# Optimization experiments

Hardware: AMD Instinct MI355X
Metric: run time of the kernel (lower is better)

## Reference

```python
import jax, jax.numpy as jnp
import numpy as np

N, E, D, H = 50000, 800000, 64, 64  # nodes, edges, feat dim, hidden dim
EPS = 1e-3  # Keras BatchNormalization default epsilon

def bn(x, g, b, mu, v):
    # inference-mode batch norm with moving statistics
    return (x - mu) * jax.lax.rsqrt(v + EPS) * g + b

def gelu(x):
    return jax.nn.gelu(x, approximate=False)  # tf.nn.gelu default is exact

def setup_inputs() -> dict:
    key = jax.random.key(0)
    ks = jax.random.split(key, 24)
    r = lambda i, shape, s=1.0: (jax.random.normal(ks[i], shape, jnp.float32) * s)
    inp = {
        "node_feats": r(0, (N, D)),
        "edge_feats": r(1, (E, D)),
        "src": jax.random.randint(ks[2], (E,), 0, N, jnp.int32),
        "dst": jax.random.randint(ks[3], (E,), 0, N, jnp.int32),
        # message MLP (BN -> Dense(gelu)) x2, input D
        "m_g1": 1.0 + 0.1 * r(4, (D,)), "m_b1": 0.1 * r(5, (D,)),
        "m_mu1": 0.1 * r(6, (D,)), "m_v1": jnp.ones((D,), jnp.float32),
        "m_W1": r(7, (D, H), 1.0 / np.sqrt(D)), "m_c1": jnp.zeros((H,), jnp.float32),
        "m_g2": 1.0 + 0.1 * r(8, (H,)), "m_b2": 0.1 * r(9, (H,)),
        "m_mu2": 0.1 * r(10, (H,)), "m_v2": jnp.ones((H,), jnp.float32),
        "m_W2": r(11, (H, H), 1.0 / np.sqrt(H)), "m_c2": jnp.zeros((H,), jnp.float32),
        # edge transformer MLP (Dense(gelu)) x2, input D
        "e_W1": r(12, (D, H), 1.0 / np.sqrt(D)), "e_c1": jnp.zeros((H,), jnp.float32),
        "e_W2": r(13, (H, H), 1.0 / np.sqrt(H)), "e_c2": jnp.zeros((H,), jnp.float32),
        # update MLP (BN -> Dense(gelu)) x2, input D+H (concat combination)
        "u_g1": 1.0 + 0.1 * r(14, (D + H,)), "u_b1": 0.1 * r(15, (D + H,)),
        "u_mu1": 0.1 * r(16, (D + H,)), "u_v1": jnp.ones((D + H,), jnp.float32),
        "u_W1": r(17, (D + H, H), 1.0 / np.sqrt(D + H)), "u_c1": jnp.zeros((H,), jnp.float32),
        "u_g2": 1.0 + 0.1 * r(18, (H,)), "u_b2": 0.1 * r(19, (H,)),
        "u_mu2": 0.1 * r(20, (H,)), "u_v2": jnp.ones((H,), jnp.float32),
        "u_W2": r(21, (H, H), 1.0 / np.sqrt(H)), "u_c2": jnp.zeros((H,), jnp.float32),
    }
    return inp

def reference(node_feats, edge_feats,
              m_g1, m_b1, m_mu1, m_v1, m_W1, m_c1,
              m_g2, m_b2, m_mu2, m_v2, m_W2, m_c2,
              e_W1, e_c1, e_W2, e_c2,
              u_g1, u_b1, u_mu1, u_v1, u_W1, u_c1,
              u_g2, u_b2, u_mu2, u_v2, u_W2, u_c2,
              src, dst):
    # gather neighbour representations: [E, D]
    nbr = node_feats[dst]
    # base message MLP: (BN -> Dropout(identity at inference) -> Dense gelu) x2
    h = gelu(bn(nbr, m_g1, m_b1, m_mu1, m_v1) @ m_W1 + m_c1)
    msg = gelu(bn(h, m_g2, m_b2, m_mu2, m_v2) @ m_W2 + m_c2)
    # edge transformer: Dense(gelu) x2, gates the messages elementwise
    er = gelu(edge_feats @ e_W1 + e_c1)
    er = gelu(er @ e_W2 + e_c2)
    msg = msg * er  # [E, H]
    # unsorted_segment_mean over source node indices (empty segments -> 0)
    s = jax.ops.segment_sum(msg, src, num_segments=N)
    cnt = jax.ops.segment_sum(jnp.ones((E, 1), msg.dtype), src, num_segments=N)
    agg = s / jnp.maximum(cnt, 1.0)  # [N, H]
    # combine ('concat') and update MLP
    hcat = jnp.concatenate([node_feats, agg], axis=-1)  # [N, D+H]
    h = gelu(bn(hcat, u_g1, u_b1, u_mu1, u_v1) @ u_W1 + u_c1)
    out = gelu(bn(h, u_g2, u_b2, u_mu2, u_v2) @ u_W2 + u_c2)
    return out  # [N, H]
```

## Files before the change

### kernel.cpp

```cpp
#include <hip/hip_runtime.h>
#include <hip/hip_bf16.h>

#define NN 50000
#define NE 800000

typedef __bf16 bf16_t;
typedef bf16_t bf16x8 __attribute__((ext_vector_type(8)));
typedef float f32x4 __attribute__((ext_vector_type(4)));

__device__ __forceinline__ float gelu_f(float x) {
    float v = x * fmaf(x * x, 0.07135481627f, 1.595769122f);
    float e = __expf(-v);
    return x * __builtin_amdgcn_rcpf(1.0f + e);
}

__device__ void fold_frag(int K, const float* W, const float* g, const float* b,
                          const float* mu, const float* v, const float* c,
                          bf16_t* Wf, float* cb, int n) {
    float acc = c[n];
    const int nt = n >> 4, lrow = n & 15, nkc = K >> 5;
    for (int k = 0; k < K; ++k) {
        float w = W[k * 64 + n];
        float s = 1.0f, o = 0.0f;
        if (g) {
            s = g[k] * __frsqrt_rn(v[k] + 1e-3f);
            o = b[k] - mu[k] * s;
        }
        int idx = ((nt * nkc + (k >> 5)) * 64 + ((k >> 3) & 3) * 16 + lrow) * 8 + (k & 7);
        Wf[idx] = (bf16_t)(w * s);
        acc += o * w;
    }
    cb[n] = acc;
}

__global__ void fold_kernel(
    const float* mg1, const float* mb1, const float* mmu1, const float* mv1,
    const float* mW1, const float* mc1,
    const float* mg2, const float* mb2, const float* mmu2, const float* mv2,
    const float* mW2, const float* mc2,
    const float* eW1, const float* ec1, const float* eW2, const float* ec2,
    const float* ug1, const float* ub1, const float* umu1, const float* uv1,
    const float* uW1, const float* uc1,
    const float* ug2, const float* ub2, const float* umu2, const float* uv2,
    const float* uW2, const float* uc2,
    bf16_t* wcat,
    bf16_t* uW1f, bf16_t* uW2f,
    float* cm1, float* cm2, float* ce1, float* ce2, float* cu1, float* cu2)
{
    int n = threadIdx.x;
    if (n >= 64) return;
    switch (blockIdx.x) {
        case 0: fold_frag(64,  mW1, mg1, mb1, mmu1, mv1, mc1, wcat,         cm1, n); break;
        case 1: fold_frag(64,  mW2, mg2, mb2, mmu2, mv2, mc2, wcat + 4096,  cm2, n); break;
        case 2: fold_frag(64,  eW1, nullptr, nullptr, nullptr, nullptr, ec1, wcat + 8192,  ce1, n); break;
        case 3: fold_frag(64,  eW2, nullptr, nullptr, nullptr, nullptr, ec2, wcat + 12288, ce2, n); break;
        case 4: fold_frag(128, uW1, ug1, ub1, umu1, uv1, uc1, uW1f, cu1, n); break;
        case 5: fold_frag(64,  uW2, ug2, ub2, umu2, uv2, uc2, uW2f, cu2, n); break;
    }
}

__device__ __forceinline__ void mk_frag_hilo(const float* row, int quad,
        bf16x8& hi0, bf16x8& lo0, bf16x8& hi1, bf16x8& lo1)
{
    #pragma unroll
    for (int j = 0; j < 8; ++j) {
        float x0 = row[quad * 8 + j];
        float x1 = row[32 + quad * 8 + j];
        bf16_t h0 = (bf16_t)x0, h1 = (bf16_t)x1;
        hi0[j] = h0; lo0[j] = (bf16_t)(x0 - (float)h0);
        hi1[j] = h1; lo1[j] = (bf16_t)(x1 - (float)h1);
    }
}

__device__ __forceinline__ bf16x8 ldb(const bf16_t* wf, int slot, int lane) {
    return *(const bf16x8*)(wf + (slot * 64 + lane) * 8);
}

__device__ __forceinline__ void gemm64_hilo(const bf16_t* wf, int m,
        bf16x8 h0, bf16x8 l0, bf16x8 h1, bf16x8 l1, f32x4 (&acc)[4], int lane)
{
    #pragma unroll
    for (int nt = 0; nt < 4; ++nt) {
        bf16x8 b0 = ldb(wf, m * 8 + nt * 2 + 0, lane);
        bf16x8 b1 = ldb(wf, m * 8 + nt * 2 + 1, lane);
        f32x4 c = {0.f, 0.f, 0.f, 0.f};
        c = __builtin_amdgcn_mfma_f32_16x16x32_bf16(h0, b0, c, 0, 0, 0);
        c = __builtin_amdgcn_mfma_f32_16x16x32_bf16(l0, b0, c, 0, 0, 0);
        c = __builtin_amdgcn_mfma_f32_16x16x32_bf16(h1, b1, c, 0, 0, 0);
        c = __builtin_amdgcn_mfma_f32_16x16x32_bf16(l1, b1, c, 0, 0, 0);
        acc[nt] = c;
    }
}

__device__ __forceinline__ void gemm64(const bf16_t* wf, int m,
        bf16x8 a0, bf16x8 a1, f32x4 (&acc)[4], int lane)
{
    #pragma unroll
    for (int nt = 0; nt < 4; ++nt) {
        bf16x8 b0 = ldb(wf, m * 8 + nt * 2 + 0, lane);
        bf16x8 b1 = ldb(wf, m * 8 + nt * 2 + 1, lane);
        f32x4 c = {0.f, 0.f, 0.f, 0.f};
        c = __builtin_amdgcn_mfma_f32_16x16x32_bf16(a0, b0, c, 0, 0, 0);
        c = __builtin_amdgcn_mfma_f32_16x16x32_bf16(a1, b1, c, 0, 0, 0);
        acc[nt] = c;
    }
}

__device__ __forceinline__ void epi_to_frag(const f32x4 (&acc)[4], const float* bias,
        bf16_t* h, int lrow, int quad)
{
    #pragma unroll
    for (int nt = 0; nt < 4; ++nt) {
        float bb = bias[nt * 16 + lrow];
        #pragma unroll
        for (int r = 0; r < 4; ++r)
            h[((nt * 2 + (lrow >> 3)) * 16 + quad * 4 + r) * 8 + (lrow & 7)] =
                (bf16_t)gelu_f(acc[nt][r] + bb);
    }
}

__global__ __launch_bounds__(256) void edge_kernel(
    const float* __restrict__ node_feats, const float* __restrict__ edge_feats,
    const int* __restrict__ src, const int* __restrict__ dst,
    const bf16_t* __restrict__ wcat,
    const float* __restrict__ cm1, const float* __restrict__ cm2,
    const float* __restrict__ ce1, const float* __restrict__ ce2,
    float* __restrict__ s_acc, int* __restrict__ cnt)
{
    __shared__ bf16_t wf[16384];
    __shared__ bf16_t hf[4][1024];

    const int tid  = threadIdx.x;
    const int wave = tid >> 6;
    const int lane = tid & 63;
    const int quad = lane >> 4;
    const int lrow = lane & 15;

    #pragma unroll
    for (int i = 0; i < 8; ++i) {
        int chunk = tid + i * 256;
        *(bf16x8*)(wf + chunk * 8) = *(const bf16x8*)(wcat + chunk * 8);
    }
    __syncthreads();

    const int ebase = blockIdx.x * 64 + wave * 16;
    bf16_t* h = hf[wave];

    if (quad == 0) atomicAdd(&cnt[src[ebase + lrow]], 1);

    f32x4 acc[4];

    {
        const float* erow = edge_feats + (size_t)(ebase + lrow) * 64;
        bf16x8 h0, l0, h1, l1;
        mk_frag_hilo(erow, quad, h0, l0, h1, l1);
        gemm64_hilo(wf, 2, h0, l0, h1, l1, acc, lane);
        epi_to_frag(acc, ce1, h, lrow, quad);
    }
    float er[4][4];
    {
        bf16x8 a0 = *(const bf16x8*)(h + lane * 8);
        bf16x8 a1 = *(const bf16x8*)(h + (lane + 64) * 8);
        gemm64(wf, 3, a0, a1, acc, lane);
        #pragma unroll
        for (int nt = 0; nt < 4; ++nt) {
            float bb = ce2[nt * 16 + lrow];
            #pragma unroll
            for (int r = 0; r < 4; ++r) er[nt][r] = gelu_f(acc[nt][r] + bb);
        }
    }

    {
        const int dnode = dst[ebase + lrow];
        const float* nrow = node_feats + (size_t)dnode * 64;
        bf16x8 h0, l0, h1, l1;
        mk_frag_hilo(nrow, quad, h0, l0, h1, l1);
        gemm64_hilo(wf, 0, h0, l0, h1, l1, acc, lane);
        epi_to_frag(acc, cm1, h, lrow, quad);
    }
    float msg[4][4];
    {
        bf16x8 a0 = *(const bf16x8*)(h + lane * 8);
        bf16x8 a1 = *(const bf16x8*)(h + (lane + 64) * 8);
        gemm64(wf, 1, a0, a1, acc, lane);
        #pragma unroll
        for (int nt = 0; nt < 4; ++nt) {
            float bb = cm2[nt * 16 + lrow];
            #pragma unroll
            for (int r = 0; r < 4; ++r) msg[nt][r] = gelu_f(acc[nt][r] + bb);
        }
    }

    #pragma unroll
    for (int r = 0; r < 4; ++r) {
        float* srow = s_acc + (size_t)src[ebase + quad * 4 + r] * 64;
        #pragma unroll
        for (int nt = 0; nt < 4; ++nt)
            unsafeAtomicAdd(srow + nt * 16 + lrow, msg[nt][r] * er[nt][r]);
    }
}

__global__ __launch_bounds__(256) void node_kernel(
    const float* __restrict__ node_feats,
    const float* __restrict__ s_acc, const int* __restrict__ cnt,
    const bf16_t* __restrict__ uW1f, const float* __restrict__ cu1,
    const bf16_t* __restrict__ uW2f, const float* __restrict__ cu2,
    float* __restrict__ out)
{
    __shared__ bf16_t w1f[8192];
    __shared__ bf16_t w2f[4096];
    __shared__ bf16_t hf[4][1024];

    const int tid  = threadIdx.x;
    const int wave = tid >> 6;
    const int lane = tid & 63;
    const int quad = lane >> 4;
    const int lrow = lane & 15;

    #pragma unroll
    for (int i = 0; i < 4; ++i) {
        int chunk = tid + i * 256;
        *(bf16x8*)(w1f + chunk * 8) = *(const bf16x8*)(uW1f + chunk * 8);
    }
    #pragma unroll
    for (int i = 0; i < 2; ++i) {
        int chunk = tid + i * 256;
        *(bf16x8*)(w2f + chunk * 8) = *(const bf16x8*)(uW2f + chunk * 8);
    }
    __syncthreads();

    const int nbase = blockIdx.x * 64 + wave * 16;
    int arow = nbase + lrow;
    arow = arow < NN ? arow : NN - 1;

    const float* nf   = node_feats + (size_t)arow * 64;
    const float* srow = s_acc + (size_t)arow * 64;
    float inv = 1.0f / fmaxf((float)cnt[arow], 1.0f);

    bf16x8 ah[4], al[4];
    #pragma unroll
    for (int j = 0; j < 8; ++j) {
        float x0 = nf[quad * 8 + j];
        float x1 = nf[32 + quad * 8 + j];
        float x2 = srow[quad * 8 + j] * inv;
        float x3 = srow[32 + quad * 8 + j] * inv;
        bf16_t h0 = (bf16_t)x0, h1 = (bf16_t)x1, h2 = (bf16_t)x2, h3 = (bf16_t)x3;
        ah[0][j] = h0; al[0][j] = (bf16_t)(x0 - (float)h0);
        ah[1][j] = h1; al[1][j] = (bf16_t)(x1 - (float)h1);
        ah[2][j] = h2; al[2][j] = (bf16_t)(x2 - (float)h2);
        ah[3][j] = h3; al[3][j] = (bf16_t)(x3 - (float)h3);
    }

    f32x4 acc[4];
    #pragma unroll
    for (int nt = 0; nt < 4; ++nt) {
        f32x4 c = {0.f, 0.f, 0.f, 0.f};
        #pragma unroll
        for (int kk = 0; kk < 4; ++kk) {
            bf16x8 b = *(const bf16x8*)(w1f + ((nt * 4 + kk) * 64 + lane) * 8);
            c = __builtin_amdgcn_mfma_f32_16x16x32_bf16(ah[kk], b, c, 0, 0, 0);
            c = __builtin_amdgcn_mfma_f32_16x16x32_bf16(al[kk], b, c, 0, 0, 0);
        }
        acc[nt] = c;
    }
    bf16_t* hb = hf[wave];
    epi_to_frag(acc, cu1, hb, lrow, quad);

    bf16x8 ha0 = *(const bf16x8*)(hb + lane * 8);
    bf16x8 ha1 = *(const bf16x8*)(hb + (lane + 64) * 8);
    gemm64(w2f, 0, ha0, ha1, acc, lane);

    #pragma unroll
    for (int nt = 0; nt < 4; ++nt) {
        int col = nt * 16 + lrow;
        float bb = cu2[col];
        #pragma unroll
        for (int r = 0; r < 4; ++r) {
            int row = nbase + quad * 4 + r;
            if (row < NN)
                out[(size_t)row * 64 + col] = gelu_f(acc[nt][r] + bb);
        }
    }
}

extern "C" void kernel_launch(void* const* d_in, const int* in_sizes, int n_in,
                              void* d_out, int out_size, void* d_ws, size_t ws_size,
                              hipStream_t stream) {
    const float* node_feats = (const float*)d_in[0];
    const float* edge_feats = (const float*)d_in[1];
    const int*   src        = (const int*)d_in[2];
    const int*   dst        = (const int*)d_in[3];

    char* ws = (char*)d_ws;
    const size_t S_BYTES = (size_t)NN * 64 * 4;
    const size_t C_BYTES = (size_t)NN * 4;
    float* s_acc = (float*)ws;
    int*   cnt   = (int*)(ws + S_BYTES);
    size_t off = S_BYTES + C_BYTES;
    bf16_t* wcat = (bf16_t*)(ws + off); off += 32768;
    bf16_t* uW1f = (bf16_t*)(ws + off); off += 16384;
    bf16_t* uW2f = (bf16_t*)(ws + off); off += 8192;
    float* cm1 = (float*)(ws + off); off += 256;
    float* cm2 = (float*)(ws + off); off += 256;
    float* ce1 = (float*)(ws + off); off += 256;
    float* ce2 = (float*)(ws + off); off += 256;
    float* cu1 = (float*)(ws + off); off += 256;
    float* cu2 = (float*)(ws + off); off += 256;

    hipMemsetAsync(s_acc, 0, S_BYTES + C_BYTES, stream);

    fold_kernel<<<6, 64, 0, stream>>>(
        (const float*)d_in[4],  (const float*)d_in[5],  (const float*)d_in[6],  (const float*)d_in[7],
        (const float*)d_in[8],  (const float*)d_in[9],
        (const float*)d_in[10], (const float*)d_in[11], (const float*)d_in[12], (const float*)d_in[13],
        (const float*)d_in[14], (const float*)d_in[15],
        (const float*)d_in[16], (const float*)d_in[17], (const float*)d_in[18], (const float*)d_in[19],
        (const float*)d_in[20], (const float*)d_in[21], (const float*)d_in[22], (const float*)d_in[23],
        (const float*)d_in[24], (const float*)d_in[25],
        (const float*)d_in[26], (const float*)d_in[27], (const float*)d_in[28], (const float*)d_in[29],
        (const float*)d_in[30], (const float*)d_in[31],
        wcat, uW1f, uW2f, cm1, cm2, ce1, ce2, cu1, cu2);

    edge_kernel<<<NE / 64, 256, 0, stream>>>(
        node_feats, edge_feats, src, dst,
        wcat, cm1, cm2, ce1, ce2, s_acc, cnt);

    node_kernel<<<(NN + 63) / 64, 256, 0, stream>>>(
        node_feats, s_acc, cnt, uW1f, cu1, uW2f, cu2, (float*)d_out);
}
```

Baseline: 547.4 us.

## Replace float atomic scatter with CSR build and deterministic per-node gather aggregation

Builds a CSR index by source node (histogram, three-pass scan, fill) and has the edge kernel write bf16 per-edge messages to a buffer instead of doing float atomics into node rows. A new per-node gather kernel sums each node's messages and divides by degree, and the update kernel then reads the precomputed mean. The fold kernel now splits the K loop across 256 threads. The goal is to remove contended global float atomics, at the cost of about 100MB of extra traffic, several extra launches, bf16 rounding of messages, and a path that only runs when the workspace is large enough.

```diff
diff --git a/kernel.cpp b/kernel.cpp
--- a/kernel.cpp
+++ b/kernel.cpp
@@ -16,10 +16,12 @@
 
 __device__ void fold_frag(int K, const float* W, const float* g, const float* b,
                           const float* mu, const float* v, const float* c,
-                          bf16_t* Wf, float* cb, int n) {
-    float acc = c[n];
+                          bf16_t* Wf, float* cb, int tid, float* part) {
+    const int n = tid & 63, kc = tid >> 6;
     const int nt = n >> 4, lrow = n & 15, nkc = K >> 5;
-    for (int k = 0; k < K; ++k) {
+    const int kq = K >> 2, k0 = kc * kq, k1 = k0 + kq;
+    float acc = 0.f;
+    for (int k = k0; k < k1; ++k) {
         float w = W[k * 64 + n];
         float s = 1.0f, o = 0.0f;
         if (g) {
@@ -30,7 +32,9 @@
         Wf[idx] = (bf16_t)(w * s);
         acc += o * w;
     }
-    cb[n] = acc;
+    part[kc * 64 + n] = acc;
+    __syncthreads();
+    if (kc == 0) cb[n] = c[n] + part[n] + part[64 + n] + part[128 + n] + part[192 + n];
 }
 
 __global__ void fold_kernel(
@@ -43,19 +47,73 @@
     const float* uW1, const float* uc1,
     const float* ug2, const float* ub2, const float* umu2, const float* uv2,
     const float* uW2, const float* uc2,
-    bf16_t* wcat,
-    bf16_t* uW1f, bf16_t* uW2f,
+    bf16_t* wcat, bf16_t* uW1f, bf16_t* uW2f,
     float* cm1, float* cm2, float* ce1, float* ce2, float* cu1, float* cu2)
 {
-    int n = threadIdx.x;
-    if (n >= 64) return;
+    __shared__ float part[256];
+    int t = threadIdx.x;
     switch (blockIdx.x) {
-        case 0: fold_frag(64,  mW1, mg1, mb1, mmu1, mv1, mc1, wcat,         cm1, n); break;
-        case 1: fold_frag(64,  mW2, mg2, mb2, mmu2, mv2, mc2, wcat + 4096,  cm2, n); break;
-        case 2: fold_frag(64,  eW1, nullptr, nullptr, nullptr, nullptr, ec1, wcat + 8192,  ce1, n); break;
-        case 3: fold_frag(64,  eW2, nullptr, nullptr, nullptr, nullptr, ec2, wcat + 12288, ce2, n); break;
-        case 4: fold_frag(128, uW1, ug1, ub1, umu1, uv1, uc1, uW1f, cu1, n); break;
-        case 5: fold_frag(64,  uW2, ug2, ub2, umu2, uv2, uc2, uW2f, cu2, n); break;
+        case 0: fold_frag(64,  mW1, mg1, mb1, mmu1, mv1, mc1, wcat,         cm1, t, part); break;
+        case 1: fold_frag(64,  mW2, mg2, mb2, mmu2, mv2, mc2, wcat + 4096,  cm2, t, part); break;
+        case 2: fold_frag(64,  eW1, nullptr, nullptr, nullptr, nullptr, ec1, wcat + 8192,  ce1, t, part); break;
+        case 3: fold_frag(64,  eW2, nullptr, nullptr, nullptr, nullptr, ec2, wcat + 12288, ce2, t, part); break;
+        case 4: fold_frag(128, uW1, ug1, ub1, umu1, uv1, uc1, uW1f, cu1, t, part); break;
+        case 5: fold_frag(64,  uW2, ug2, ub2, umu2, uv2, uc2, uW2f, cu2, t, part); break;
+    }
+}
+
+__global__ void hist_kernel(const int* __restrict__ src, int* __restrict__ cnt) {
+    int e = blockIdx.x * 256 + threadIdx.x;
+    if (e < NE) atomicAdd(&cnt[src[e]], 1);
+}
+
+__global__ void scanA_kernel(const int* __restrict__ cnt, int* __restrict__ part,
+                             int* __restrict__ btot) {
+    __shared__ int s[256];
+    int tid = threadIdx.x;
+    int i = blockIdx.x * 256 + tid;
+    int v = (i < NN) ? cnt[i] : 0;
+    s[tid] = v;
+    __syncthreads();
+    #pragma unroll
+    for (int off = 1; off < 256; off <<= 1) {
+        int t = (tid >= off) ? s[tid - off] : 0;
+        __syncthreads();
+        s[tid] += t;
+        __syncthreads();
+    }
+    if (i < NN) part[i] = s[tid] - v;
+    if (tid == 255) btot[blockIdx.x] = s[255];
+}
+
+__global__ void scanB_kernel(int* __restrict__ btot, int nblk) {
+    __shared__ int s[256];
+    int tid = threadIdx.x;
+    int v = (tid < nblk) ? btot[tid] : 0;
+    s[tid] = v;
+    __syncthreads();
+    #pragma unroll
+    for (int off = 1; off < 256; off <<= 1) {
+        int t = (tid >= off) ? s[tid - off] : 0;
+        __syncthreads();
+        s[tid] += t;
+        __syncthreads();
+    }
+    if (tid < nblk) btot[tid] = s[tid] - v;
+}
+
+__global__ void scanC_kernel(const int* __restrict__ part, const int* __restrict__ btot,
+                             int* __restrict__ woff) {
+    int i = blockIdx.x * 256 + threadIdx.x;
+    if (i < NN) woff[i] = part[i] + btot[i >> 8];
+}
+
+__global__ void fill_kernel(const int* __restrict__ src, int* __restrict__ woff,
+                            int* __restrict__ elist) {
+    int e = blockIdx.x * 256 + threadIdx.x;
+    if (e < NE) {
+        int pos = atomicAdd(&woff[src[e]], 1);
+        elist[pos] = e;
     }
 }
 
@@ -125,7 +183,7 @@
     const bf16_t* __restrict__ wcat,
     const float* __restrict__ cm1, const float* __restrict__ cm2,
     const float* __restrict__ ce1, const float* __restrict__ ce2,
-    float* __restrict__ s_acc, int* __restrict__ cnt)
+    float* __restrict__ s_acc, bf16_t* __restrict__ buf, int use_csr)
 {
     __shared__ bf16_t wf[16384];
     __shared__ bf16_t hf[4][1024];
@@ -145,8 +203,6 @@
 
     const int ebase = blockIdx.x * 64 + wave * 16;
     bf16_t* h = hf[wave];
-
-    if (quad == 0) atomicAdd(&cnt[src[ebase + lrow]], 1);
 
     f32x4 acc[4];
 
@@ -191,18 +247,56 @@
         }
     }
 
-    #pragma unroll
-    for (int r = 0; r < 4; ++r) {
-        float* srow = s_acc + (size_t)src[ebase + quad * 4 + r] * 64;
-        #pragma unroll
-        for (int nt = 0; nt < 4; ++nt)
-            unsafeAtomicAdd(srow + nt * 16 + lrow, msg[nt][r] * er[nt][r]);
-    }
-}
-
-__global__ __launch_bounds__(256) void node_kernel(
+    if (use_csr) {
+        #pragma unroll
+        for (int r = 0; r < 4; ++r) {
+            bf16_t* bp = buf + (size_t)(ebase + quad * 4 + r) * 64;
+            #pragma unroll
+            for (int nt = 0; nt < 4; ++nt)
+                bp[nt * 16 + lrow] = (bf16_t)(msg[nt][r] * er[nt][r]);
+        }
+    } else {
+        #pragma unroll
+        for (int r = 0; r < 4; ++r) {
+            float* srow = s_acc + (size_t)src[ebase + quad * 4 + r] * 64;
+            #pragma unroll
+            for (int nt = 0; nt < 4; ++nt)
+                unsafeAtomicAdd(srow + nt * 16 + lrow, msg[nt][r] * er[nt][r]);
+        }
+    }
+}
+
+__global__ __launch_bounds__(256) void agg_kernel(
+    const bf16_t* __restrict__ buf, const int* __restrict__ elist,
+    const int* __restrict__ woff, const int* __restrict__ cnt,
+    float* __restrict__ agg)
+{
+    const int wave = threadIdx.x >> 6;
+    const int lane = threadIdx.x & 63;
+    const int n = blockIdx.x * 4 + wave;
+    const int deg = cnt[n];
+    const int end = woff[n];
+    const int start = end - deg;
+
+    float s0 = 0.f, s1 = 0.f, s2 = 0.f, s3 = 0.f;
+    int j = start;
+    for (; j + 4 <= end; j += 4) {
+        int e0 = elist[j], e1 = elist[j + 1], e2 = elist[j + 2], e3 = elist[j + 3];
+        s0 += (float)buf[(size_t)e0 * 64 + lane];
+        s1 += (float)buf[(size_t)e1 * 64 + lane];
+        s2 += (float)buf[(size_t)e2 * 64 + lane];
+        s3 += (float)buf[(size_t)e3 * 64 + lane];
+    }
+    for (; j < end; ++j)
+        s0 += (float)buf[(size_t)elist[j] * 64 + lane];
+
+    float r = (deg > 0) ? (s0 + s1 + s2 + s3) * __builtin_amdgcn_rcpf((float)deg) : 0.f;
+    agg[(size_t)n * 64 + lane] = r;
+}
+
+__global__ __launch_bounds__(256) void update_kernel(
     const float* __restrict__ node_feats,
-    const float* __restrict__ s_acc, const int* __restrict__ cnt,
+    const float* __restrict__ aggv, const int* __restrict__ cnt,
     const bf16_t* __restrict__ uW1f, const float* __restrict__ cu1,
     const bf16_t* __restrict__ uW2f, const float* __restrict__ cu2,
     float* __restrict__ out)
@@ -234,8 +328,8 @@
     arow = arow < NN ? arow : NN - 1;
 
     const float* nf   = node_feats + (size_t)arow * 64;
-    const float* srow = s_acc + (size_t)arow * 64;
-    float inv = 1.0f / fmaxf((float)cnt[arow], 1.0f);
+    const float* srow = aggv + (size_t)arow * 64;
+    float inv = cnt ? 1.0f / fmaxf((float)cnt[arow], 1.0f) : 1.0f;
 
     bf16x8 ah[4], al[4];
     #pragma unroll
@@ -292,11 +386,25 @@
     const int*   dst        = (const int*)d_in[3];
 
     char* ws = (char*)d_ws;
-    const size_t S_BYTES = (size_t)NN * 64 * 4;
-    const size_t C_BYTES = (size_t)NN * 4;
-    float* s_acc = (float*)ws;
-    int*   cnt   = (int*)(ws + S_BYTES);
-    size_t off = S_BYTES + C_BYTES;
+    const bool csr = ws_size >= (size_t)119200000;
+
+    size_t off = 0;
+    bf16_t* buf = nullptr; float* agg = nullptr; int* elist = nullptr;
+    int* cnt = nullptr; int* woff = nullptr; int* part = nullptr; int* btot = nullptr;
+    float* s_acc = nullptr;
+
+    if (csr) {
+        buf   = (bf16_t*)(ws + off); off += (size_t)NE * 64 * 2;
+        agg   = (float*)(ws + off);  off += (size_t)NN * 64 * 4;
+        elist = (int*)(ws + off);    off += (size_t)NE * 4;
+        cnt   = (int*)(ws + off);    off += (size_t)NN * 4;
+        woff  = (int*)(ws + off);    off += (size_t)NN * 4;
+        part  = (int*)(ws + off);    off += (size_t)NN * 4;
+        btot  = (int*)(ws + off);    off += 1024;
+    } else {
+        s_acc = (float*)(ws + off);  off += (size_t)NN * 64 * 4;
+        cnt   = (int*)(ws + off);    off += (size_t)NN * 4;
+    }
     bf16_t* wcat = (bf16_t*)(ws + off); off += 32768;
     bf16_t* uW1f = (bf16_t*)(ws + off); off += 16384;
     bf16_t* uW2f = (bf16_t*)(ws + off); off += 8192;
@@ -307,9 +415,13 @@
     float* cu1 = (float*)(ws + off); off += 256;
     float* cu2 = (float*)(ws + off); off += 256;
 
-    hipMemsetAsync(s_acc, 0, S_BYTES + C_BYTES, stream);
-
-    fold_kernel<<<6, 64, 0, stream>>>(
+    if (csr) {
+        hipMemsetAsync(cnt, 0, (size_t)NN * 4, stream);
+    } else {
+        hipMemsetAsync(s_acc, 0, (size_t)NN * 64 * 4 + (size_t)NN * 4, stream);
+    }
+
+    fold_kernel<<<6, 256, 0, stream>>>(
         (const float*)d_in[4],  (const float*)d_in[5],  (const float*)d_in[6],  (const float*)d_in[7],
         (const float*)d_in[8],  (const float*)d_in[9],
         (const float*)d_in[10], (const float*)d_in[11], (const float*)d_in[12], (const float*)d_in[13],
@@ -321,10 +433,26 @@
         (const float*)d_in[30], (const float*)d_in[31],
         wcat, uW1f, uW2f, cm1, cm2, ce1, ce2, cu1, cu2);
 
+    hist_kernel<<<(NE + 255) / 256, 256, 0, stream>>>(src, cnt);
+
+    if (csr) {
+        const int NBLK = (NN + 255) / 256;
+        scanA_kernel<<<NBLK, 256, 0, stream>>>(cnt, part, btot);
+        scanB_kernel<<<1, 256, 0, stream>>>(btot, NBLK);
+        scanC_kernel<<<NBLK, 256, 0, stream>>>(part, btot, woff);
+        fill_kernel<<<(NE + 255) / 256, 256, 0, stream>>>(src, woff, elist);
+    }
+
     edge_kernel<<<NE / 64, 256, 0, stream>>>(
         node_feats, edge_feats, src, dst,
-        wcat, cm1, cm2, ce1, ce2, s_acc, cnt);
-
-    node_kernel<<<(NN + 63) / 64, 256, 0, stream>>>(
-        node_feats, s_acc, cnt, uW1f, cu1, uW2f, cu2, (float*)d_out);
-}
+        wcat, cm1, cm2, ce1, ce2, s_acc, buf, csr ? 1 : 0);
+
+    if (csr) {
+        agg_kernel<<<NN / 4, 256, 0, stream>>>(buf, elist, woff, cnt, agg);
+        update_kernel<<<(NN + 63) / 64, 256, 0, stream>>>(
+            node_feats, agg, nullptr, uW1f, cu1, uW2f, cu2, (float*)d_out);
+    } else {
+        update_kernel<<<(NN + 63) / 64, 256, 0, stream>>>(
+            node_feats, s_acc, cnt, uW1f, cu1, uW2f, cu2, (float*)d_out);
+    }
+}
```

After: 563.5 us. +2.9%, slower.
